# Kernel tuning notes

Hardware: AMD Instinct MI355X
Metric: run time of the kernel (lower is better)

Reference implementation:

```python
import jax, jax.numpy as jnp
import numpy as np

PACK = 8  # 32 bits / 4 bits per value


def _unpack_int4(packed):
    # packed: [..., O//8] int32 -> [..., O] int32 nibbles in [0, 16)
    shifts = jnp.arange(PACK, dtype=jnp.int32) * 4
    nib = (packed[..., None] >> shifts) & jnp.int32(0xF)
    return nib.reshape(*packed.shape[:-1], packed.shape[-1] * PACK)


def setup_inputs() -> dict:
    key = jax.random.key(0)
    k1, k2, k3, k4 = jax.random.split(key, 4)
    I, O, GS = 4096, 11008, 128
    G = I // GS
    x = jax.random.normal(k1, (4096, I), dtype=jnp.float32)
    qweight = jax.random.randint(k2, (I, O // PACK), -2**31, 2**31 - 1, dtype=jnp.int32)
    scales = jax.random.uniform(k3, (G, O), dtype=jnp.float32) * 0.01 + 1e-3
    qzeros = jax.random.randint(k4, (G, O // PACK), -2**31, 2**31 - 1, dtype=jnp.int32)
    return {"x": x, "qweight": qweight, "scales": scales, "qzeros": qzeros, "group_size": GS}


def reference(x, qweight, scales, qzeros, group_size):
    I = qweight.shape[0]
    O = qweight.shape[1] * PACK
    G = I // group_size
    w_int = _unpack_int4(qweight)                       # [I, O] int32
    z_int = _unpack_int4(qzeros)                        # [G, O] int32
    # dequant: (w - zero_of_group) * scale_of_group
    w_grp = w_int.reshape(G, group_size, O).astype(jnp.float32)
    w_deq = (w_grp - z_int[:, None, :].astype(jnp.float32)) * scales[:, None, :]
    w_deq = w_deq.reshape(I, O)                         # [I, O] float32
    return x @ w_deq                                    # [N, O]
```

## Files before the change

### kernel.cpp

```cpp
#include <hip/hip_runtime.h>
#include <hip/hip_bf16.h>
#include <stdint.h>

#define M_DIM 4096
#define K_DIM 4096
#define N_DIM 11008
#define OPACK (N_DIM / 8)
#define GSZ   128

#define NIT 32

typedef __attribute__((ext_vector_type(8))) short short8;
typedef __attribute__((ext_vector_type(4))) float floatx4;
typedef __attribute__((ext_vector_type(4))) unsigned int uintx4;

static __device__ __forceinline__ unsigned short f32_to_bf16_rne(float f) {
    union { float f; unsigned int u; } c; c.f = f;
    unsigned int u = c.u;
    u += 0x7fffu + ((u >> 16) & 1u);
    return (unsigned short)(u >> 16);
}

static __device__ __forceinline__ void load16_lds(const void* gptr, void* lptr) {
    __builtin_amdgcn_global_load_lds(
        (__attribute__((address_space(1))) void*)gptr,
        (__attribute__((address_space(3))) void*)lptr,
        16, 0, 0);
}

__global__ __launch_bounds__(256)
void convert_x_kernel(const float* __restrict__ x, unsigned short* __restrict__ xb) {
    const int idx = (blockIdx.x * 256 + threadIdx.x) * 8;
    floatx4 v0 = *(const floatx4*)(x + idx);
    floatx4 v1 = *(const floatx4*)(x + idx + 4);
    unsigned short r[8];
#pragma unroll
    for (int i = 0; i < 4; i++) {
        r[i]     = f32_to_bf16_rne(v0[i]);
        r[4 + i] = f32_to_bf16_rne(v1[i]);
    }
    *(uintx4*)(xb + idx) = *(const uintx4*)r;
}

__global__ __launch_bounds__(256)
void dequant_kernel(const int* __restrict__ qweight, const float* __restrict__ scales,
                    const int* __restrict__ qzeros, unsigned short* __restrict__ Wt) {
    const int o  = blockIdx.x * 256 + threadIdx.x;
    const int i0 = blockIdx.y * 64;
    const int g  = i0 >> 7;
    const int op = o >> 3;
    const int sh = (o & 7) * 4;
    const int z  = (qzeros[g * OPACK + op] >> sh) & 15;
    const float s = scales[g * N_DIM + o];
    unsigned short buf[64];
#pragma unroll
    for (int k = 0; k < 64; k++) {
        const int q   = qweight[(i0 + k) * OPACK + op];
        const float w = (float)(((q >> sh) & 15) - z) * s;
        buf[k] = f32_to_bf16_rne(w);
    }
    uintx4* dst = (uintx4*)(Wt + (size_t)o * K_DIM + i0);
    const uintx4* src = (const uintx4*)buf;
#pragma unroll
    for (int t = 0; t < 8; t++) dst[t] = src[t];
}


#define STAGE_A(KB, RG) do {                                   \
    const char* g_ = ApS + (size_t)(KB) * 64;                  \
    char* l_ = (char*)lds_a[RG] + tid * 16;                    \
    load16_lds(g_, l_);                                        \
    load16_lds(g_ + (1u << 20), l_ + 8192);                    \
} while (0)

#define STAGE_B(KB, RG) do {                                   \
    const char* g_ = BpS + (size_t)(KB) * 64;                  \
    char* l_ = (char*)lds_b[RG] + tid * 16;                    \
    load16_lds(g_, l_);                                        \
    load16_lds(g_ + (1u << 20), l_ + 8192);                    \
} while (0)

#define VM_NONE ((void)0)
#define VM_TILE do {                                                        \
    if (more) { asm volatile("s_waitcnt vmcnt(6)" ::: "memory"); }          \
    else      { asm volatile("s_waitcnt vmcnt(0)" ::: "memory"); }          \
} while (0)

#define PHASE(B_, KS_, H_, VMW_, ...) do {                                           \
    const short* Ar_ = &lds_a[(B_) * 2 + (KS_)][a_off + (H_) * 2048];                \
    short8 av_[4];                                                                   \
    _Pragma("unroll")                                                                \
    for (int f_ = 0; f_ < 4; ++f_) av_[f_] = *(const short8*)(Ar_ + f_ * 512);       \
    if ((H_) == 0) {                                                                 \
        const short* Br_ = &lds_b[(B_) * 2 + (KS_)][b_off];                          \
        _Pragma("unroll")                                                            \
        for (int n_ = 0; n_ < 4; ++n_) bv[n_] = *(const short8*)(Br_ + n_ * 512);    \
    }                                                                                \
    __VA_ARGS__;                                                                     \
    VMW_;                                                                            \
    __builtin_amdgcn_s_barrier();                                                    \
    asm volatile("s_waitcnt lgkmcnt(0)" ::: "memory");                               \
    __builtin_amdgcn_sched_barrier(0);                                               \
    __builtin_amdgcn_s_setprio(1);                                                   \
    _Pragma("unroll")                                                                \
    for (int f_ = 0; f_ < 4; ++f_)                                                   \
        _Pragma("unroll")                                                            \
        for (int n_ = 0; n_ < 4; ++n_)                                               \
            acc[(H_) * 4 + f_][n_] = __builtin_amdgcn_mfma_f32_16x16x32_bf16(        \
                av_[f_], bv[n_], acc[(H_) * 4 + f_][n_], 0, 0, 0);                   \
    __builtin_amdgcn_s_setprio(0);                                                   \
    __builtin_amdgcn_s_barrier();                                                    \
} while (0)

__global__ __launch_bounds__(512, 2)
void gemm_kernel(const unsigned short* __restrict__ X,
                 const unsigned short* __restrict__ Wt,
                 float* __restrict__ C) {
    __shared__ __align__(16) short lds_a[4][8192];
    __shared__ __align__(16) short lds_b[4][8192];

    const int tid  = threadIdx.x;
    const int wave = tid >> 6;
    const int lane = tid & 63;
    const int wm   = wave >> 2;
    const int wn   = wave & 3;

    const int pid    = blockIdx.x;
    const int L      = (pid & 7) * 86 + (pid >> 3);
    const int m_tile = L & 15;
    const int n_tile = L >> 4;
    const int m0 = m_tile * 256;
    const int n0 = n_tile * 256;

    const int row_l = tid >> 2;
    const int cl    = (tid & 3) ^ ((tid >> 3) & 3);
    const char* ApS = (const char*)X  + ((size_t)(m0 + row_l) << 13) + (cl << 4);
    const char* BpS = (const char*)Wt + ((size_t)(n0 + row_l) << 13) + (cl << 4);

    const int l15 = lane & 15;
    const int kcs = (lane >> 4) ^ ((lane >> 1) & 3);
    const int a_off = (wm * 128 + l15) * 32 + kcs * 8;
    const int b_off = (wn * 64  + l15) * 32 + kcs * 8;

    floatx4 acc[8][4] = {};
    short8 bv[4];

    STAGE_B(0, 0); STAGE_A(0, 0);
    STAGE_B(1, 1); STAGE_A(1, 1);
    STAGE_B(2, 2); STAGE_A(2, 2);
    STAGE_B(3, 3);
    asm volatile("s_waitcnt vmcnt(6)" ::: "memory");
    __builtin_amdgcn_s_barrier();

#pragma unroll 1
    for (int i = 0; i < NIT; ++i) {
        const int  kb4  = 4 * i;
        const bool more = (i + 1 < NIT);
        PHASE(0, 0, 0, VM_NONE, STAGE_A(kb4 + 3, 3));
        PHASE(0, 0, 1, VM_NONE, if (more) STAGE_B(kb4 + 4, 0));
        PHASE(0, 1, 0, VM_NONE, if (more) STAGE_A(kb4 + 4, 0));
        PHASE(0, 1, 1, VM_TILE, if (more) STAGE_B(kb4 + 5, 1));
        PHASE(1, 0, 0, VM_NONE, if (more) STAGE_A(kb4 + 5, 1));
        PHASE(1, 0, 1, VM_NONE, if (more) STAGE_B(kb4 + 6, 2));
        PHASE(1, 1, 0, VM_NONE, if (more) STAGE_A(kb4 + 6, 2));
        PHASE(1, 1, 1, VM_TILE, if (more) STAGE_B(kb4 + 7, 3));
    }

    const int crow = (lane >> 4) * 4;
#pragma unroll
    for (int f = 0; f < 8; ++f) {
#pragma unroll
        for (int n = 0; n < 4; ++n) {
            float* Cp = C + (size_t)(m0 + wm * 128 + f * 16 + crow) * N_DIM
                          + (n0 + wn * 64 + n * 16 + l15);
#pragma unroll
            for (int r = 0; r < 4; ++r)
                __builtin_nontemporal_store(acc[f][n][r], Cp + (size_t)r * N_DIM);
        }
    }
}

extern "C" void kernel_launch(void* const* d_in, const int* in_sizes, int n_in,
                              void* d_out, int out_size, void* d_ws, size_t ws_size,
                              hipStream_t stream) {
    const float* x       = (const float*)d_in[0];
    const int*   qweight = (const int*)d_in[1];
    const float* scales  = (const float*)d_in[2];
    const int*   qzeros  = (const int*)d_in[3];
    float* out = (float*)d_out;

    unsigned short* Xb = (unsigned short*)d_ws;
    unsigned short* Wt = (unsigned short*)((char*)d_ws + (size_t)M_DIM * K_DIM * 2);

    convert_x_kernel<<<(M_DIM * K_DIM) / (256 * 8), 256, 0, stream>>>(x, Xb);
    dequant_kernel<<<dim3(N_DIM / 256, K_DIM / 64), 256, 0, stream>>>(qweight, scales, qzeros, Wt);
    gemm_kernel<<<(M_DIM / 256) * (N_DIM / 256), 512, 0, stream>>>(Xb, Wt, out);
}
```

Before: 620.3 us.

## Prefetch next phase LDS fragments after MFMA block, one barrier per phase

Restructures the GEMM main loop so each phase issues its MFMAs on fragments already held in registers, then waits on vmcnt, reads the next phase's A/B fragments from LDS, issues the next global-to-LDS stage, and hits a single barrier. This removes the second barrier per phase and the lgkmcnt(0) stall that came before the MFMAs, aiming to overlap LDS reads with MFMA execution. The vmcnt waits are moved and tightened (vmcnt(4) at finer granularity), and the explicit ordering relies on the asm barrier and waitcnt placement. That placement risks races if the compiler reorders the LDS reads, and it raises register pressure because fragments are kept live across phases.

```diff
diff --git a/kernel.cpp b/kernel.cpp
--- a/kernel.cpp
+++ b/kernel.cpp
@@ -80,36 +80,36 @@
     load16_lds(g_ + (1u << 20), l_ + 8192);                    \
 } while (0)
 
+#define VM4 asm volatile("s_waitcnt vmcnt(4)" ::: "memory")
+#define VM0 asm volatile("s_waitcnt vmcnt(0)" ::: "memory")
 #define VM_NONE ((void)0)
-#define VM_TILE do {                                                        \
-    if (more) { asm volatile("s_waitcnt vmcnt(6)" ::: "memory"); }          \
-    else      { asm volatile("s_waitcnt vmcnt(0)" ::: "memory"); }          \
-} while (0)
-
-#define PHASE(B_, KS_, H_, VMW_, ...) do {                                           \
-    const short* Ar_ = &lds_a[(B_) * 2 + (KS_)][a_off + (H_) * 2048];                \
-    short8 av_[4];                                                                   \
-    _Pragma("unroll")                                                                \
-    for (int f_ = 0; f_ < 4; ++f_) av_[f_] = *(const short8*)(Ar_ + f_ * 512);       \
-    if ((H_) == 0) {                                                                 \
-        const short* Br_ = &lds_b[(B_) * 2 + (KS_)][b_off];                          \
-        _Pragma("unroll")                                                            \
-        for (int n_ = 0; n_ < 4; ++n_) bv[n_] = *(const short8*)(Br_ + n_ * 512);    \
-    }                                                                                \
-    __VA_ARGS__;                                                                     \
-    VMW_;                                                                            \
-    __builtin_amdgcn_s_barrier();                                                    \
-    asm volatile("s_waitcnt lgkmcnt(0)" ::: "memory");                               \
-    __builtin_amdgcn_sched_barrier(0);                                               \
+
+#define LDA_FRAGS(RG_, RH_) do {                                                  \
+    const short* Ar_ = &lds_a[RG_][a_off + (RH_) * 2048];                         \
+    _Pragma("unroll")                                                             \
+    for (int f_ = 0; f_ < 4; ++f_) av[f_] = *(const short8*)(Ar_ + f_ * 512);     \
+} while (0)
+
+#define LDB_FRAGS(RG_) do {                                                       \
+    const short* Br_ = &lds_b[RG_][b_off];                                        \
+    _Pragma("unroll")                                                             \
+    for (int n_ = 0; n_ < 4; ++n_) bv[n_] = *(const short8*)(Br_ + n_ * 512);     \
+} while (0)
+
+#define PHASE(H_, RG_, RH_, LB_, RDC_, VMW_, STG_) do {                              \
     __builtin_amdgcn_s_setprio(1);                                                   \
     _Pragma("unroll")                                                                \
     for (int f_ = 0; f_ < 4; ++f_)                                                   \
         _Pragma("unroll")                                                            \
         for (int n_ = 0; n_ < 4; ++n_)                                               \
             acc[(H_) * 4 + f_][n_] = __builtin_amdgcn_mfma_f32_16x16x32_bf16(        \
-                av_[f_], bv[n_], acc[(H_) * 4 + f_][n_], 0, 0, 0);                   \
+                av[f_], bv[n_], acc[(H_) * 4 + f_][n_], 0, 0, 0);                    \
     __builtin_amdgcn_s_setprio(0);                                                   \
-    __builtin_amdgcn_s_barrier();                                                    \
+    __builtin_amdgcn_sched_barrier(0);                                               \
+    VMW_;                                                                            \
+    if (RDC_) { LDA_FRAGS(RG_, RH_); if (LB_) LDB_FRAGS(RG_); }                      \
+    STG_;                                                                            \
+    asm volatile("s_barrier" ::: "memory");                                          \
 } while (0)
 
 __global__ __launch_bounds__(512, 2)
@@ -143,27 +143,29 @@
     const int b_off = (wn * 64  + l15) * 32 + kcs * 8;
 
     floatx4 acc[8][4] = {};
-    short8 bv[4];
+    short8 av[4], bv[4];
 
     STAGE_B(0, 0); STAGE_A(0, 0);
     STAGE_B(1, 1); STAGE_A(1, 1);
     STAGE_B(2, 2); STAGE_A(2, 2);
     STAGE_B(3, 3);
     asm volatile("s_waitcnt vmcnt(6)" ::: "memory");
-    __builtin_amdgcn_s_barrier();
+    asm volatile("s_barrier" ::: "memory");
+    LDA_FRAGS(0, 0);
+    LDB_FRAGS(0);
 
 #pragma unroll 1
     for (int i = 0; i < NIT; ++i) {
         const int  kb4  = 4 * i;
         const bool more = (i + 1 < NIT);
-        PHASE(0, 0, 0, VM_NONE, STAGE_A(kb4 + 3, 3));
-        PHASE(0, 0, 1, VM_NONE, if (more) STAGE_B(kb4 + 4, 0));
-        PHASE(0, 1, 0, VM_NONE, if (more) STAGE_A(kb4 + 4, 0));
-        PHASE(0, 1, 1, VM_TILE, if (more) STAGE_B(kb4 + 5, 1));
-        PHASE(1, 0, 0, VM_NONE, if (more) STAGE_A(kb4 + 5, 1));
-        PHASE(1, 0, 1, VM_NONE, if (more) STAGE_B(kb4 + 6, 2));
-        PHASE(1, 1, 0, VM_NONE, if (more) STAGE_A(kb4 + 6, 2));
-        PHASE(1, 1, 1, VM_TILE, if (more) STAGE_B(kb4 + 7, 3));
+        PHASE(0, 0, 1, 0, 1, VM_NONE,                  STAGE_A(kb4 + 3, 3));
+        PHASE(1, 1, 0, 1, 1, VM4,                      if (more) STAGE_B(kb4 + 4, 0));
+        PHASE(0, 1, 1, 0, 1, VM_NONE,                  if (more) STAGE_A(kb4 + 4, 0));
+        PHASE(1, 2, 0, 1, 1, if (more) VM4; else VM0,  if (more) STAGE_B(kb4 + 5, 1));
+        PHASE(0, 2, 1, 0, 1, VM_NONE,                  if (more) STAGE_A(kb4 + 5, 1));
+        PHASE(1, 3, 0, 1, 1, if (more) VM4,            if (more) STAGE_B(kb4 + 6, 2));
+        PHASE(0, 3, 1, 0, 1, VM_NONE,                  if (more) STAGE_A(kb4 + 6, 2));
+        PHASE(1, 0, 0, 1, more, if (more) VM4,         if (more) STAGE_B(kb4 + 7, 3));
     }
 
     const int crow = (lane >> 4) * 4;
```

Result: no change. 616.1 us (-0.7%).
